# Kernel tuning notes

Measured on AMD Instinct MI355X. Metric: run time of the kernel, lower is better.

The kernel has to match this reference:

```python
import jax, jax.numpy as jnp
import numpy as np

EPS = 1e-5

def adain_norm(x):
    # per-(batch,channel) instance normalization over spatial dims (AdaIN projection)
    mean = jnp.mean(x, axis=(2, 3), keepdims=True)
    var = jnp.var(x, axis=(2, 3), keepdims=True)
    return (x - mean) / jnp.sqrt(var + EPS)

def conv1x1(x, w, b):
    # x: [B,C,H,W], w: [O,C], b: [O]
    return jnp.einsum('bchw,oc->bohw', x, w) + b[None, :, None, None]

def setup_inputs() -> dict:
    key = jax.random.key(0)
    ks = jax.random.split(key, 10)
    B, C, H, W = 4, 512, 64, 64
    s = 1.0 / np.sqrt(C)
    return {
        'x': jax.random.normal(ks[0], (B, C, H, W), jnp.float32),
        'y': jax.random.normal(ks[1], (B, C, H, W), jnp.float32),
        'f_w': jax.random.normal(ks[2], (C, C), jnp.float32) * s,
        'f_b': jnp.zeros((C,), jnp.float32),
        'g_w': jax.random.normal(ks[3], (C, C), jnp.float32) * s,
        'g_b': jnp.zeros((C,), jnp.float32),
        'h_w': jax.random.normal(ks[4], (C, C), jnp.float32) * s,
        'h_b': jnp.zeros((C,), jnp.float32),
        'out_w': jax.random.normal(ks[5], (C, C), jnp.float32) * s,
        'out_b': jnp.zeros((C,), jnp.float32),
    }

def reference(x, y, f_w, f_b, g_w, g_b, h_w, h_b, out_w, out_b):
    B, C, H, W = x.shape
    HW = H * W
    xn = adain_norm(x)
    yn = adain_norm(y)
    # 1x1 conv projections, flattened over spatial dims
    f = conv1x1(xn, f_w, f_b).reshape(B, C, HW)   # [B,C,HWx]
    g = conv1x1(yn, g_w, g_b).reshape(B, C, HW)   # [B,C,HWy]
    energy = jnp.einsum('bci,bcj->bij', f, g)     # [B,HWx,HWy]
    correlation = jax.nn.softmax(energy, axis=-1)
    h = conv1x1(y, h_w, h_b).reshape(B, C, HW)    # [B,C,HWy]
    # residual = h @ correlation^T -> [B,C,HWx]
    residual = jnp.einsum('bcj,bij->bci', h, correlation).reshape(B, C, H, W)
    residual = conv1x1(residual, out_w, out_b)
    return x + residual
```

## Files before the change

kernel.cpp:

```cpp
#include <hip/hip_runtime.h>
#include <stdint.h>

#define HW 4096
#define NC 512
#define NB 4

typedef __attribute__((ext_vector_type(8))) _Float16 f16x8;
typedef __attribute__((ext_vector_type(4))) float f32x4;
typedef __attribute__((ext_vector_type(4))) unsigned short ush4;
typedef __attribute__((ext_vector_type(8))) unsigned short ush8;

typedef __attribute__((address_space(1))) const void* as1_cvp;
typedef __attribute__((address_space(3))) void* as3_vp;

__device__ __forceinline__ unsigned short f2h(float f) {
  union { _Float16 h; unsigned short u; } c;
  c.h = (_Float16)f;
  return c.u;
}

__global__ __launch_bounds__(256) void moments_k(const float* __restrict__ x,
                                                 const float* __restrict__ y,
                                                 float* __restrict__ stats) {
  int bid = blockIdx.x;
  int tens = bid >> 11;
  int row = bid & 2047;
  const float* src = (tens ? y : x) + (size_t)row * HW;
  float s = 0.f, s2 = 0.f;
  for (int j = threadIdx.x; j < HW / 4; j += 256) {
    float4 v = ((const float4*)src)[j];
    s += (v.x + v.y) + (v.z + v.w);
    s2 += (v.x * v.x + v.y * v.y) + (v.z * v.z + v.w * v.w);
  }
  #pragma unroll
  for (int o = 32; o; o >>= 1) { s += __shfl_down(s, o); s2 += __shfl_down(s2, o); }
  __shared__ float rs[8];
  int w = threadIdx.x >> 6;
  if ((threadIdx.x & 63) == 0) { rs[w] = s; rs[4 + w] = s2; }
  __syncthreads();
  if (threadIdx.x == 0) {
    float S = (rs[0] + rs[1]) + (rs[2] + rs[3]);
    float S2 = (rs[4] + rs[5]) + (rs[6] + rs[7]);
    float mean = S * (1.f / HW);
    float var = S2 * (1.f / HW) - mean * mean;
    stats[tens * 4096 + row] = mean;
    stats[tens * 4096 + 2048 + row] = rsqrtf(var + 1e-5f);
  }
}

__global__ __launch_bounds__(256) void transnorm_k(const float* __restrict__ x,
                                                   const float* __restrict__ y,
                                                   const float* __restrict__ stats,
                                                   unsigned short* __restrict__ xnT,
                                                   unsigned short* __restrict__ ynT,
                                                   unsigned short* __restrict__ yT) {
  __shared__ float tile[64][65];
  int zi = blockIdx.z;
  int b = zi / 3, mode = zi - b * 3;
  int i0 = blockIdx.x * 64, c0 = blockIdx.y * 64;
  const float* src = (mode == 0 ? x : y);
  unsigned short* dst = (mode == 0 ? xnT : (mode == 1 ? ynT : yT));
  int t = threadIdx.x;
  int c = t >> 2;
  int isub = (t & 3) << 4;
  float mean = 0.f, rstd = 1.f;
  if (mode < 2) {
    int srow = (mode ? 4096 : 0) + b * NC + c0 + c;
    mean = stats[srow];
    rstd = stats[srow + 2048];
  }
  const float4* sp = (const float4*)(src + ((size_t)(b * NC + c0 + c)) * HW + i0 + isub);
  #pragma unroll
  for (int k = 0; k < 4; ++k) {
    float4 v = sp[k];
    int ib = isub + k * 4;
    tile[ib + 0][c] = (v.x - mean) * rstd;
    tile[ib + 1][c] = (v.y - mean) * rstd;
    tile[ib + 2][c] = (v.z - mean) * rstd;
    tile[ib + 3][c] = (v.w - mean) * rstd;
  }
  __syncthreads();
  int i = t >> 2;
  int cc = (t & 3) << 4;
  unsigned short* op = dst + ((size_t)b * HW + i0 + i) * NC + c0 + cc;
  #pragma unroll
  for (int h = 0; h < 2; ++h) {
    ush8 o;
    #pragma unroll
    for (int e = 0; e < 8; ++e) o[e] = f2h(tile[i][cc + h * 8 + e]);
    *(ush8*)(op + h * 8) = o;
  }
}

__global__ __launch_bounds__(256) void castw_k(const float* __restrict__ fw,
                                               const float* __restrict__ gw,
                                               const float* __restrict__ hw_,
                                               const float* __restrict__ ow,
                                               unsigned short* __restrict__ dst) {
  int idx = blockIdx.x * 256 + threadIdx.x;
  int which = idx >> 16;
  int sub = idx & 65535;
  const float* s = which == 0 ? fw : which == 1 ? gw : which == 2 ? hw_ : ow;
  float4 v = ((const float4*)s)[sub];
  ush4 o;
  o[0] = f2h(v.x); o[1] = f2h(v.y); o[2] = f2h(v.z); o[3] = f2h(v.w);
  *(ush4*)(dst + (size_t)idx * 4) = o;
}

__global__ __launch_bounds__(256) void softmax_k(float* __restrict__ S) {
  float* row = S + (size_t)blockIdx.x * HW;
  int t = threadIdx.x;
  float4 v[4];
  float mx = -3.0e38f;
  #pragma unroll
  for (int r = 0; r < 4; ++r) {
    v[r] = ((const float4*)row)[r * 256 + t];
    mx = fmaxf(mx, fmaxf(fmaxf(v[r].x, v[r].y), fmaxf(v[r].z, v[r].w)));
  }
  #pragma unroll
  for (int o = 32; o; o >>= 1) mx = fmaxf(mx, __shfl_down(mx, o));
  __shared__ float red[8];
  int w = t >> 6;
  if ((t & 63) == 0) red[w] = mx;
  __syncthreads();
  mx = fmaxf(fmaxf(red[0], red[1]), fmaxf(red[2], red[3]));
  float sum = 0.f;
  #pragma unroll
  for (int r = 0; r < 4; ++r) {
    v[r].x = __expf(v[r].x - mx);
    v[r].y = __expf(v[r].y - mx);
    v[r].z = __expf(v[r].z - mx);
    v[r].w = __expf(v[r].w - mx);
    sum += (v[r].x + v[r].y) + (v[r].z + v[r].w);
  }
  #pragma unroll
  for (int o = 32; o; o >>= 1) sum += __shfl_down(sum, o);
  if ((t & 63) == 0) red[4 + w] = sum;
  __syncthreads();
  float inv = 1.f / ((red[4] + red[5]) + (red[6] + red[7]));
  unsigned short* orow = (unsigned short*)row;
  #pragma unroll
  for (int r = 0; r < 4; ++r) {
    ush4 o;
    o[0] = f2h(v[r].x * inv);
    o[1] = f2h(v[r].y * inv);
    o[2] = f2h(v[r].z * inv);
    o[3] = f2h(v[r].w * inv);
    *(ush4*)(orow + ((size_t)(r * 256 + t)) * 4) = o;
  }
}

__global__ __launch_bounds__(256) void reduce_k(const float* __restrict__ S,
                                                unsigned short* __restrict__ op,
                                                long long PSo, int nsplit, int R, int pzs) {
  int e = blockIdx.x * 256 + threadIdx.x;
  int bg = e >> pzs;
  int rem = e - (bg << pzs);
  int m = rem >> 7;
  int c4 = rem & 127;
  const float* rowp = S + (size_t)bg * R * HW + (size_t)m * HW + 2048 + c4 * 4;
  float4 s = {0.f, 0.f, 0.f, 0.f};
  for (int sp = 0; sp < nsplit; ++sp) {
    float4 v = *(const float4*)(rowp + sp * 512);
    s.x += v.x; s.y += v.y; s.z += v.z; s.w += v.w;
  }
  ush4 o;
  o[0] = f2h(s.x); o[1] = f2h(s.y); o[2] = f2h(s.z); o[3] = f2h(s.w);
  *(ush4*)(op + (size_t)bg * PSo + (size_t)m * NC + c4 * 4) = o;
}

__global__ __launch_bounds__(256) void gemm_nt(
    const unsigned short* __restrict__ A, long long sA, int lda,
    const unsigned short* __restrict__ Bm, long long sB, int ldb,
    void* __restrict__ Cp, long long sC, long long sCs, int ldc,
    int K, int out_f32, int ls,
    const float* __restrict__ bias_m, const float* __restrict__ bias_n,
    const float* __restrict__ add_src, long long sAdd) {
  __shared__ short lsA[128 * 64];
  __shared__ short lsB[128 * 64];
  const int t = threadIdx.x;
  const int lane = t & 63;
  const int w = t >> 6;
  const int wm = w >> 1, wn = w & 1;
  const long long bz = blockIdx.z;
  const long long bg = bz >> ls;
  const int sp = (int)(bz - (bg << ls));
  const long long koff = (long long)sp * K;
  const unsigned short* Ab = A + bg * sA + koff + (size_t)blockIdx.x * 128 * lda;
  const unsigned short* Bb = Bm + bg * sB + koff + (size_t)blockIdx.y * 128 * ldb;

  f32x4 zero = {0.f, 0.f, 0.f, 0.f};
  f32x4 acc[4][4];
  #pragma unroll
  for (int i = 0; i < 4; ++i)
    #pragma unroll
    for (int j = 0; j < 4; ++j) acc[i][j] = zero;

  const int nkt = K >> 6;
  for (int kt = 0; kt < nkt; ++kt) {
    const int kbase = kt << 6;
    #pragma unroll
    for (int i = 0; i < 4; ++i) {
      int q = t + i * 256;
      int r = q >> 3, xx = q & 7;
      int gk = kbase + ((xx ^ (r & 7)) << 3);
      __builtin_amdgcn_global_load_lds((as1_cvp)(const void*)(Ab + (size_t)r * lda + gk),
                                       (as3_vp)(void*)(&lsA[q << 3]), 16, 0, 0);
      __builtin_amdgcn_global_load_lds((as1_cvp)(const void*)(Bb + (size_t)r * ldb + gk),
                                       (as3_vp)(void*)(&lsB[q << 3]), 16, 0, 0);
    }
    __syncthreads();
    #pragma unroll
    for (int ks = 0; ks < 2; ++ks) {
      f16x8 av[4], bv[4];
      const int xl = ks * 4 + (lane >> 4);
      const int rr = lane & 15;
      #pragma unroll
      for (int mb = 0; mb < 4; ++mb) {
        int row = wm * 64 + mb * 16 + rr;
        av[mb] = *(const f16x8*)&lsA[(row << 6) + ((xl ^ (row & 7)) << 3)];
      }
      #pragma unroll
      for (int nb = 0; nb < 4; ++nb) {
        int row = wn * 64 + nb * 16 + rr;
        bv[nb] = *(const f16x8*)&lsB[(row << 6) + ((xl ^ (row & 7)) << 3)];
      }
      #pragma unroll
      for (int mb = 0; mb < 4; ++mb)
        #pragma unroll
        for (int nb = 0; nb < 4; ++nb)
          acc[mb][nb] = __builtin_amdgcn_mfma_f32_16x16x32_f16(av[mb], bv[nb], acc[mb][nb], 0, 0, 0);
    }
    __syncthreads();
  }

  const int mb0 = blockIdx.x * 128 + wm * 64;
  const int nb0 = blockIdx.y * 128 + wn * 64;
  const int cn = lane & 15;
  const int rq = (lane >> 4) << 2;
  float* cf = (float*)Cp;
  unsigned short* ch = (unsigned short*)Cp;
  #pragma unroll
  for (int mb = 0; mb < 4; ++mb) {
    #pragma unroll
    for (int nb = 0; nb < 4; ++nb) {
      int n = nb0 + nb * 16 + cn;
      float bn = bias_n ? bias_n[n] : 0.f;
      #pragma unroll
      for (int r = 0; r < 4; ++r) {
        int m = mb0 + mb * 16 + rq + r;
        float vv = acc[mb][nb][r] + bn;
        if (bias_m) vv += bias_m[m];
        if (add_src) vv += add_src[bg * sAdd + (size_t)m * ldc + n];
        size_t off = (size_t)(bg * sC) + (size_t)sp * sCs + (size_t)m * ldc + n;
        if (out_f32) cf[off] = vv;
        else ch[off] = f2h(vv);
      }
    }
  }
}

extern "C" void kernel_launch(void* const* d_in, const int* in_sizes, int n_in,
                              void* d_out, int out_size, void* d_ws, size_t ws_size,
                              hipStream_t stream) {
  const float* x = (const float*)d_in[0];
  const float* y = (const float*)d_in[1];
  const float* f_w = (const float*)d_in[2];
  const float* f_b = (const float*)d_in[3];
  const float* g_w = (const float*)d_in[4];
  const float* g_b = (const float*)d_in[5];
  const float* h_w = (const float*)d_in[6];
  const float* h_b = (const float*)d_in[7];
  const float* out_w = (const float*)d_in[8];
  const float* out_b = (const float*)d_in[9];
  float* out = (float*)d_out;

  char* ws = (char*)d_ws;
  size_t off = 0;
  auto alloc = [&](size_t bytes) -> char* {
    char* p = ws + off;
    off += (bytes + 255) & ~(size_t)255;
    return p;
  };
  const size_t TN = (size_t)NB * HW * NC;
  float* stats = (float*)alloc(8192 * sizeof(float));
  unsigned short* wB = (unsigned short*)alloc((size_t)4 * 512 * 512 * 2);
  unsigned short* xnT = (unsigned short*)alloc(TN * 2);
  unsigned short* ynT = (unsigned short*)alloc(TN * 2);
  unsigned short* yT = (unsigned short*)alloc(TN * 2);
  unsigned short* fB = (unsigned short*)alloc(TN * 2);
  unsigned short* gB = (unsigned short*)alloc(TN * 2);
  unsigned short* hB = (unsigned short*)alloc(TN * 2);
  unsigned short* oB = xnT;
  size_t remain = ws_size > off ? ws_size - off : 0;
  const size_t SB = (size_t)HW * HW * 4;
  int G, nsplit, R = HW;
  if (remain >= 4 * SB)      { G = 4; nsplit = 1; }
  else if (remain >= 2 * SB) { G = 2; nsplit = 2; }
  else if (remain >= SB)     { G = 1; nsplit = 4; }
  else {
    G = 1; nsplit = 4;
    while (R > 128 && (size_t)R * HW * 4 > remain) R >>= 1;
  }
  const int lsplit = (nsplit == 4) ? 2 : (nsplit == 2 ? 1 : 0);
  float* S = (float*)alloc((size_t)G * R * HW * 4);
  if (off > ws_size) return;

  castw_k<<<dim3(1024), dim3(256), 0, stream>>>(f_w, g_w, h_w, out_w, wB);
  moments_k<<<dim3(4096), dim3(256), 0, stream>>>(x, y, stats);
  transnorm_k<<<dim3(64, 8, 12), dim3(256), 0, stream>>>(x, y, stats, xnT, ynT, yT);

  const long long PS = (long long)HW * NC;
  gemm_nt<<<dim3(32, 4, NB), dim3(256), 0, stream>>>(xnT, PS, NC, wB, 0, NC,
                                                     fB, PS, 0, NC, NC, 0, 0,
                                                     nullptr, f_b, nullptr, 0);
  gemm_nt<<<dim3(32, 4, NB), dim3(256), 0, stream>>>(ynT, PS, NC, wB + 262144, 0, NC,
                                                     gB, PS, 0, NC, NC, 0, 0,
                                                     nullptr, g_b, nullptr, 0);
  gemm_nt<<<dim3(4, 32, NB), dim3(256), 0, stream>>>(wB + 524288, 0, NC, yT, PS, NC,
                                                     hB, PS, 0, HW, NC, 0, 0,
                                                     h_b, nullptr, nullptr, 0);

  const int Ksplit = HW / nsplit;
  const int pzs = 31 - __builtin_clz((unsigned)(R * (NC / 4)));
  for (int b0 = 0; b0 < NB; b0 += G) {
    for (int r0 = 0; r0 < HW; r0 += R) {
      gemm_nt<<<dim3(R / 128, 32, G), dim3(256), 0, stream>>>(
          fB + ((size_t)b0 * HW + r0) * NC, PS, NC,
          gB + (size_t)b0 * PS, PS, NC,
          S, (long long)R * HW, 0, HW, NC, 1, 0, nullptr, nullptr, nullptr, 0);
      softmax_k<<<dim3(G * R), dim3(256), 0, stream>>>(S);
      if (nsplit > 1) {
        gemm_nt<<<dim3(R / 128, 4, G * nsplit), dim3(256), 0, stream>>>(
            (const unsigned short*)S, (long long)R * 2 * HW, 2 * HW,
            hB + (size_t)b0 * NC * HW, (long long)NC * HW, HW,
            S + 2048, (long long)R * HW, 512, HW, Ksplit, 1, lsplit,
            nullptr, nullptr, nullptr, 0);
        reduce_k<<<dim3(G * R / 2), dim3(256), 0, stream>>>(
            S, oB + ((size_t)b0 * HW + r0) * NC, PS, nsplit, R, pzs);
      } else {
        gemm_nt<<<dim3(R / 128, 4, G), dim3(256), 0, stream>>>(
            (const unsigned short*)S, (long long)R * 2 * HW, 2 * HW,
            hB + (size_t)b0 * NC * HW, (long long)NC * HW, HW,
            oB + ((size_t)b0 * HW + r0) * NC, PS, 0, NC, HW, 0, 0,
            nullptr, nullptr, nullptr, 0);
      }
    }
  }
  gemm_nt<<<dim3(4, 32, NB), dim3(256), 0, stream>>>(wB + 786432, 0, NC, oB, PS, NC,
                                                     out, (long long)NC * HW, 0, HW, NC, 1, 0,
                                                     out_b, nullptr, x, (long long)NC * HW);
}
```

Before: 465.5 us.

## Add 256x256-tile MFMA GEMM for attention energy and PV products

Adds a new 512-thread GEMM kernel with 256x256 output tiles, XOR-swizzled double-buffered LDS filled by direct global-to-LDS loads, and 16x16x32 f16 MFMAs. It is used for both the energy GEMM and the split-K correlation-times-h GEMM. The goal is more operand reuse per LDS load than the old 128-wide tiles give. The PV product now always uses a four-way K split plus a reduce pass, even when the workspace could hold a no-split layout. Each block uses 128KB of LDS, so only one block fits per CU, and the larger tiles give fewer blocks overall.

```diff
diff --git a/kernel.cpp b/kernel.cpp
--- a/kernel.cpp
+++ b/kernel.cpp
@@ -260,6 +260,105 @@
   }
 }
 
+__global__ __launch_bounds__(512, 2) void gemm_nt2(
+    const unsigned short* __restrict__ A, long long sA, int lda,
+    const unsigned short* __restrict__ Bm, long long sB, int ldb,
+    void* __restrict__ Cp, long long sC, long long sCs, int ldc,
+    int K, int out_f32, int ls,
+    const float* __restrict__ bias_n) {
+  __shared__ short lsA[2][256 * 64];
+  __shared__ short lsB[2][256 * 64];
+  const int t = threadIdx.x;
+  const int lane = t & 63;
+  const int w = t >> 6;
+  const int wm = w >> 2, wn = w & 3;
+  const long long bz = blockIdx.z;
+  const long long bg = bz >> ls;
+  const int sp = (int)(bz - (bg << ls));
+  const long long koff = (long long)sp * K;
+  const unsigned short* Ab = A + bg * sA + koff + (size_t)blockIdx.x * 256 * lda;
+  const unsigned short* Bb = Bm + bg * sB + koff + (size_t)blockIdx.y * 256 * ldb;
+
+  f32x4 zero = {0.f, 0.f, 0.f, 0.f};
+  f32x4 acc[8][4];
+  #pragma unroll
+  for (int i = 0; i < 8; ++i)
+    #pragma unroll
+    for (int j = 0; j < 4; ++j) acc[i][j] = zero;
+
+  const int rr = lane & 15;
+  const int xl = lane >> 4;
+  const int nkt = K >> 6;
+
+  auto STAGE = [&](int buf, int kt) {
+    const int kbase = kt << 6;
+    #pragma unroll
+    for (int i = 0; i < 4; ++i) {
+      int q = t + i * 512;
+      int r = q >> 3, xx = q & 7;
+      int gk = kbase + ((xx ^ (r & 7)) << 3);
+      __builtin_amdgcn_global_load_lds((as1_cvp)(const void*)(Ab + (size_t)r * lda + gk),
+                                       (as3_vp)(void*)(&lsA[buf][q << 3]), 16, 0, 0);
+      __builtin_amdgcn_global_load_lds((as1_cvp)(const void*)(Bb + (size_t)r * ldb + gk),
+                                       (as3_vp)(void*)(&lsB[buf][q << 3]), 16, 0, 0);
+    }
+  };
+
+  STAGE(0, 0);
+  __syncthreads();
+  int cur = 0;
+  for (int kt = 0; kt < nkt; ++kt) {
+    if (kt + 1 < nkt) STAGE(cur ^ 1, kt + 1);
+    #pragma unroll
+    for (int ks = 0; ks < 2; ++ks) {
+      f16x8 av[8], bv[4];
+      const int cb = ks * 4 + xl;
+      #pragma unroll
+      for (int mb = 0; mb < 8; ++mb) {
+        int row = wm * 128 + mb * 16 + rr;
+        av[mb] = *(const f16x8*)&lsA[cur][(row << 6) + ((cb ^ (row & 7)) << 3)];
+      }
+      #pragma unroll
+      for (int nb = 0; nb < 4; ++nb) {
+        int row = wn * 64 + nb * 16 + rr;
+        bv[nb] = *(const f16x8*)&lsB[cur][(row << 6) + ((cb ^ (row & 7)) << 3)];
+      }
+      __builtin_amdgcn_s_setprio(1);
+      #pragma unroll
+      for (int mb = 0; mb < 8; ++mb)
+        #pragma unroll
+        for (int nb = 0; nb < 4; ++nb)
+          acc[mb][nb] = __builtin_amdgcn_mfma_f32_16x16x32_f16(av[mb], bv[nb], acc[mb][nb], 0, 0, 0);
+      __builtin_amdgcn_s_setprio(0);
+    }
+    __syncthreads();
+    cur ^= 1;
+  }
+
+  const int mb0 = blockIdx.x * 256 + wm * 128;
+  const int nb0 = blockIdx.y * 256 + wn * 64;
+  const int cn = lane & 15;
+  const int rq = (lane >> 4) << 2;
+  float* cf = (float*)Cp;
+  unsigned short* ch = (unsigned short*)Cp;
+  #pragma unroll
+  for (int mb = 0; mb < 8; ++mb) {
+    #pragma unroll
+    for (int nb = 0; nb < 4; ++nb) {
+      int n = nb0 + nb * 16 + cn;
+      float bn = bias_n ? bias_n[n] : 0.f;
+      #pragma unroll
+      for (int r = 0; r < 4; ++r) {
+        int m = mb0 + mb * 16 + rq + r;
+        float vv = acc[mb][nb][r] + bn;
+        size_t off = (size_t)(bg * sC) + (size_t)sp * sCs + (size_t)m * ldc + n;
+        if (out_f32) cf[off] = vv;
+        else ch[off] = f2h(vv);
+      }
+    }
+  }
+}
+
 extern "C" void kernel_launch(void* const* d_in, const int* in_sizes, int n_in,
                               void* d_out, int out_size, void* d_ws, size_t ws_size,
                               hipStream_t stream) {
@@ -294,15 +393,14 @@
   unsigned short* oB = xnT;
   size_t remain = ws_size > off ? ws_size - off : 0;
   const size_t SB = (size_t)HW * HW * 4;
-  int G, nsplit, R = HW;
-  if (remain >= 4 * SB)      { G = 4; nsplit = 1; }
-  else if (remain >= 2 * SB) { G = 2; nsplit = 2; }
-  else if (remain >= SB)     { G = 1; nsplit = 4; }
+  int G, R = HW;
+  if (remain >= 4 * SB)      { G = 4; }
+  else if (remain >= 2 * SB) { G = 2; }
+  else if (remain >= SB)     { G = 1; }
   else {
-    G = 1; nsplit = 4;
+    G = 1;
     while (R > 128 && (size_t)R * HW * 4 > remain) R >>= 1;
   }
-  const int lsplit = (nsplit == 4) ? 2 : (nsplit == 2 ? 1 : 0);
   float* S = (float*)alloc((size_t)G * R * HW * 4);
   if (off > ws_size) return;
 
@@ -321,29 +419,34 @@
                                                      hB, PS, 0, HW, NC, 0, 0,
                                                      h_b, nullptr, nullptr, 0);
 
-  const int Ksplit = HW / nsplit;
   const int pzs = 31 - __builtin_clz((unsigned)(R * (NC / 4)));
   for (int b0 = 0; b0 < NB; b0 += G) {
     for (int r0 = 0; r0 < HW; r0 += R) {
-      gemm_nt<<<dim3(R / 128, 32, G), dim3(256), 0, stream>>>(
-          fB + ((size_t)b0 * HW + r0) * NC, PS, NC,
-          gB + (size_t)b0 * PS, PS, NC,
-          S, (long long)R * HW, 0, HW, NC, 1, 0, nullptr, nullptr, nullptr, 0);
-      softmax_k<<<dim3(G * R), dim3(256), 0, stream>>>(S);
-      if (nsplit > 1) {
-        gemm_nt<<<dim3(R / 128, 4, G * nsplit), dim3(256), 0, stream>>>(
+      if (R >= 256) {
+        gemm_nt2<<<dim3(R / 256, HW / 256, G), dim3(512), 0, stream>>>(
+            fB + ((size_t)b0 * HW + r0) * NC, PS, NC,
+            gB + (size_t)b0 * PS, PS, NC,
+            S, (long long)R * HW, 0, HW, NC, 1, 0, nullptr);
+        softmax_k<<<dim3(G * R), dim3(256), 0, stream>>>(S);
+        gemm_nt2<<<dim3(R / 256, NC / 256, G * 4), dim3(512), 0, stream>>>(
             (const unsigned short*)S, (long long)R * 2 * HW, 2 * HW,
             hB + (size_t)b0 * NC * HW, (long long)NC * HW, HW,
-            S + 2048, (long long)R * HW, 512, HW, Ksplit, 1, lsplit,
+            S + 2048, (long long)R * HW, 512, HW, HW / 4, 1, 2, nullptr);
+        reduce_k<<<dim3(G * R / 2), dim3(256), 0, stream>>>(
+            S, oB + ((size_t)b0 * HW + r0) * NC, PS, 4, R, pzs);
+      } else {
+        gemm_nt<<<dim3(R / 128, 32, G), dim3(256), 0, stream>>>(
+            fB + ((size_t)b0 * HW + r0) * NC, PS, NC,
+            gB + (size_t)b0 * PS, PS, NC,
+            S, (long long)R * HW, 0, HW, NC, 1, 0, nullptr, nullptr, nullptr, 0);
+        softmax_k<<<dim3(G * R), dim3(256), 0, stream>>>(S);
+        gemm_nt<<<dim3(R / 128, 4, G * 4), dim3(256), 0, stream>>>(
+            (const unsigned short*)S, (long long)R * 2 * HW, 2 * HW,
+            hB + (size_t)b0 * NC * HW, (long long)NC * HW, HW,
+            S + 2048, (long long)R * HW, 512, HW, HW / 4, 1, 2,
             nullptr, nullptr, nullptr, 0);
         reduce_k<<<dim3(G * R / 2), dim3(256), 0, stream>>>(
-            S, oB + ((size_t)b0 * HW + r0) * NC, PS, nsplit, R, pzs);
-      } else {
-        gemm_nt<<<dim3(R / 128, 4, G), dim3(256), 0, stream>>>(
-            (const unsigned short*)S, (long long)R * 2 * HW, 2 * HW,
-            hB + (size_t)b0 * NC * HW, (long long)NC * HW, HW,
-            oB + ((size_t)b0 * HW + r0) * NC, PS, 0, NC, HW, 0, 0,
-            nullptr, nullptr, nullptr, 0);
+            S, oB + ((size_t)b0 * HW + r0) * NC, PS, 4, R, pzs);
       }
     }
   }
```

New measurement: 446.5 us. 1.04x faster.
